# Kernel optimization log

Hardware: AMD Instinct MI355X
Metric: run time of the kernel (lower is better)

Reference implementation:

```python
import jax, jax.numpy as jnp
import numpy as np

B, N, C = 8, 2048, 128
K = 16
DILATIONS = (1, 2)
KMAX = K * max(DILATIONS)  # neighbors constructed by DilatedKnnGraph
NEG_SLOPE = 0.2


def setup_inputs() -> dict:
    key = jax.random.key(0)
    ks = jax.random.split(key, 12)
    D = len(DILATIONS)

    def nrm(k, shape, fan_in):
        return jax.random.normal(k, shape, jnp.float32) / np.float32(np.sqrt(fan_in))

    x = jax.random.normal(ks[0], (B, N, C), jnp.float32)
    pos = jax.random.normal(ks[1], (B, N, 3), jnp.float32)
    # PointTransformerConv params per dilation layer (bias-free lin/lin_src/lin_dst, pos_nn=Linear(3,C))
    W_lin = nrm(ks[2], (D, C, C), C)
    W_src = nrm(ks[3], (D, C, C), C)
    W_dst = nrm(ks[4], (D, C, C), C)
    W_pos = nrm(ks[5], (D, 3, C), 3)
    b_pos = jnp.zeros((D, C), jnp.float32)
    # global fusion MLP: Linear(C+3, C) + LeakyReLU(0.2)
    Wg = nrm(ks[6], (C + 3, C), C + 3)
    bg = jnp.zeros((C,), jnp.float32)
    # final MLP: Linear(C,C) + LeakyReLU(0.2) + Linear(C,3)
    W1 = nrm(ks[7], (C, C), C)
    b1 = jnp.zeros((C,), jnp.float32)
    W2 = nrm(ks[8], (C, 3), C)
    b2 = jnp.zeros((3,), jnp.float32)
    return dict(x=x, pos=pos, W_lin=W_lin, W_src=W_src, W_dst=W_dst,
                W_pos=W_pos, b_pos=b_pos, Wg=Wg, bg=bg, W1=W1, b1=b1, W2=W2, b2=b2)


def _knn(p):
    # p: [N, 3] -> [N, KMAX] neighbor indices sorted by ascending distance (self excluded)
    sq = jnp.sum(p * p, axis=-1)
    d2 = sq[:, None] + sq[None, :] - 2.0 * (p @ p.T)
    d2 = d2 + jnp.eye(p.shape[0], dtype=p.dtype) * jnp.float32(1e10)
    _, idx = jax.lax.top_k(-d2, KMAX)
    return idx


def reference(x, pos, W_lin, W_src, W_dst, W_pos, b_pos, Wg, bg, W1, b1, W2, b2):
    nbr = jax.vmap(_knn)(pos)  # [B, N, KMAX]
    self_idx = jnp.broadcast_to(jnp.arange(N)[None, :, None], (B, N, 1))
    gather = jax.vmap(lambda arr, idx: arr[idx])  # per-cloud fancy gather

    h = None
    for li, d in enumerate(DILATIONS):
        # Dilated neighbor selection: every d-th of sorted neighbors, keep K, plus self loop
        idx = jnp.concatenate([nbr[:, :, ::d][:, :, :K], self_idx], axis=-1)  # [B, N, K+1]
        pos_j = gather(pos, idx)  # [B, N, K+1, 3]
        # delta_ij = pos_nn(pos_i - pos_j)
        delta = jnp.einsum('bnkt,tc->bnkc', pos[:, :, None, :] - pos_j, W_pos[li]) + b_pos[li]
        s = x @ W_src[li]   # lin_src
        v = x @ W_lin[li]   # value projection
        t = x @ W_dst[li]   # lin_dst
        # alpha_ij = lin_dst(x_i) - lin_src(x_j) + delta ; per-channel softmax over neighbors
        alpha = t[:, :, None, :] - gather(s, idx) + delta  # [B, N, K+1, C]
        w = jax.nn.softmax(alpha, axis=2)
        h_ = jnp.sum(w * (gather(v, idx) + delta), axis=2)  # [B, N, C]
        h = h_ if h is None else h + h_

    h2 = jax.nn.leaky_relu(jnp.concatenate([x, pos], axis=-1) @ Wg + bg, NEG_SLOPE)
    h = h + h2
    res = jax.nn.leaky_relu(h @ W1 + b1, NEG_SLOPE) @ W2 + b2
    return res + pos  # add_points=True
```

## Files before the change

### kernel.cpp

```cpp
#include <hip/hip_runtime.h>

#define BB 8
#define NN 2048
#define CC 128
#define KMAX 32
#define NEG 0.2f
#define CH 8
#define CHSZ (NN / CH)
#define CAP 32

using bf16x8 = __attribute__((ext_vector_type(8))) short;
using f32x4  = __attribute__((ext_vector_type(4))) float;

__device__ __forceinline__ unsigned int f2key(float f) {
  unsigned int b = __float_as_uint(f);
  return (b & 0x80000000u) ? ~b : (b | 0x80000000u);
}

__device__ __forceinline__ float sq3(float x, float y, float z) {
  return __fadd_rn(__fadd_rn(__fmul_rn(x, x), __fmul_rn(y, y)), __fmul_rn(z, z));
}

__device__ __forceinline__ float d2np(float px, float py, float pz, float sqq,
                                      float qx, float qy, float qz, float sqj) {
  float dot = __fmaf_rn(pz, qz, __fmaf_rn(py, qy, __fmul_rn(px, qx)));
  return __fsub_rn(__fadd_rn(sqq, sqj), __fmul_rn(2.0f, dot));
}

__device__ __forceinline__ unsigned short f2bf(float f) {
  unsigned int u = __float_as_uint(f);
  return (unsigned short)((u + 0x7fffu + ((u >> 16) & 1u)) >> 16);
}
__device__ __forceinline__ float bf2f(unsigned short u) {
  return __uint_as_float(((unsigned int)u) << 16);
}

__device__ __forceinline__ bf16x8 cvt8(const float* __restrict__ p) {
  float4 a = *(const float4*)(p);
  float4 b = *(const float4*)(p + 4);
  bf16x8 r;
  r[0] = (short)f2bf(a.x); r[1] = (short)f2bf(a.y);
  r[2] = (short)f2bf(a.z); r[3] = (short)f2bf(a.w);
  r[4] = (short)f2bf(b.x); r[5] = (short)f2bf(b.y);
  r[6] = (short)f2bf(b.z); r[7] = (short)f2bf(b.w);
  return r;
}

__device__ __forceinline__ int paddr(int c, int jj) { return (c << 8) + (jj ^ c); }

__device__ __forceinline__ void knn_body(int bx, int tid,
                                         const float* __restrict__ pos,
                                         unsigned short* __restrict__ cand,
                                         unsigned int* __restrict__ candk,
                                         float4* __restrict__ sp4,
                                         unsigned char* __restrict__ sbuf) {
  int b = bx >> 6;
  int qbase = (bx & 63) * 32;
  const float* pb = pos + (size_t)b * NN * 3;
  for (int t = tid; t < NN; t += 256) {
    float xx = pb[t * 3 + 0];
    float yy = pb[t * 3 + 1];
    float zz = pb[t * 3 + 2];
    sp4[paddr(t >> 8, t & 255)] = make_float4(xx, yy, zz, sq3(xx, yy, zz));
  }
  __syncthreads();

  int q = qbase + (tid >> 3);
  int c = tid & 7;
  float4 pq = sp4[paddr(q >> 8, q & 255)];
  float px = pq.x, py = pq.y, pz = pq.z;
  float sqq = pq.w;
  int j0 = c * CHSZ;

  const float SENT = 3.0e38f;
  float a0 = SENT, a1 = SENT, a2 = SENT, a3 = SENT;
#pragma unroll 4
  for (int jj = 0; jj < CHSZ; ++jj) {
    float4 pj = sp4[paddr(c, jj)];
    float d2 = d2np(px, py, pz, sqq, pj.x, pj.y, pj.z, pj.w);
    if (j0 + jj == q) d2 = SENT;
    float m0 = fmaxf(a0, d2); a0 = fminf(a0, d2);
    float m1 = fmaxf(a1, m0); a1 = fminf(a1, m0);
    float m2 = fmaxf(a2, m1); a2 = fminf(a2, m1);
    a3 = fminf(a3, m2);
  }

  float T = a3;
  T = fmaxf(T, __shfl_xor(T, 1));
  T = fmaxf(T, __shfl_xor(T, 2));
  T = fmaxf(T, __shfl_xor(T, 4));

  unsigned int ak[KMAX];
  int ai[KMAX];
#pragma unroll
  for (int k = 0; k < KMAX; ++k) { ak[k] = 0xFFFFFFFFu; ai[k] = 0xFFFF; }

  int sbase = tid * CAP;
  auto drain = [&](int cnt2) {
    for (int u = 0; u < cnt2; ++u) {
      int jj2 = (int)sbuf[sbase + u];
      int j = j0 + jj2;
      float4 pj = sp4[paddr(c, jj2)];
      float d2 = d2np(px, py, pz, sqq, pj.x, pj.y, pj.z, pj.w);
      unsigned int key = f2key(d2);
      if (key < ak[KMAX - 1]) {
#pragma unroll
        for (int k = KMAX - 1; k >= 1; --k) {
          bool ck  = key < ak[k];
          bool ckm = key < ak[k - 1];
          unsigned int tk = ckm ? ak[k - 1] : key;
          int          ti = ckm ? ai[k - 1] : j;
          ak[k] = ck ? tk : ak[k];
          ai[k] = ck ? ti : ai[k];
        }
        bool c0b = key < ak[0];
        ak[0] = c0b ? key : ak[0];
        ai[0] = c0b ? j : ai[0];
      }
    }
  };

  int cnt = 0;
  for (int jj = 0; jj < CHSZ; ++jj) {
    float4 pj = sp4[paddr(c, jj)];
    float d2 = d2np(px, py, pz, sqq, pj.x, pj.y, pj.z, pj.w);
    bool pass = (d2 <= T) && (j0 + jj != q);
    if (pass) {
      if (cnt == CAP) { drain(CAP); cnt = 0; }
      sbuf[sbase + cnt] = (unsigned char)jj;
      ++cnt;
    }
  }
  drain(cnt);

  size_t obase = (((size_t)(b * NN + q)) * CH + c) * KMAX;
  unsigned short* oc = cand + obase;
  unsigned int* ok = candk + obase;
#pragma unroll
  for (int k = 0; k < KMAX; ++k) {
    oc[k] = (unsigned short)ai[k];
    ok[k] = ak[k];
  }
}

__device__ __forceinline__ void proj_body(int z, int mx, int tid,
                                          const float* __restrict__ x,
                                          const unsigned short* __restrict__ wf,
                                          unsigned short* __restrict__ projb) {
  unsigned short* out = projb + (size_t)z * ((size_t)BB * NN * CC);
  int wave = tid >> 6;
  int lane = tid & 63;
  int m0 = (mx * 4 + wave) * 16;
  int quad = lane >> 4;
  int am = m0 + (lane & 15);

  f32x4 acc[8];
#pragma unroll
  for (int nt = 0; nt < 8; ++nt) acc[nt] = (f32x4){0.f, 0.f, 0.f, 0.f};

  const unsigned short* wz = wf + (size_t)z * (8 * 4 * 64 * 8);
#pragma unroll
  for (int ks = 0; ks < 4; ++ks) {
    bf16x8 a = cvt8(x + (size_t)am * CC + ks * 32 + quad * 8);
#pragma unroll
    for (int nt = 0; nt < 8; ++nt) {
      bf16x8 bfr = *(const bf16x8*)(wz + (size_t)(((nt * 4 + ks) * 64 + lane) * 8));
      acc[nt] = __builtin_amdgcn_mfma_f32_16x16x32_bf16(a, bfr, acc[nt], 0, 0, 0);
    }
  }

  int col0 = lane & 15;
#pragma unroll
  for (int nt = 0; nt < 8; ++nt)
#pragma unroll
    for (int r = 0; r < 4; ++r)
      out[(size_t)(m0 + quad * 4 + r) * CC + nt * 16 + col0] = f2bf(acc[nt][r]);
}

__device__ __forceinline__ void wg_body(int mx, int tid,
                                        const float* __restrict__ x,
                                        const float* __restrict__ pos,
                                        const unsigned short* __restrict__ wf,
                                        const float* __restrict__ wgtail,
                                        const float* __restrict__ bg,
                                        float* __restrict__ h) {
  int wave = tid >> 6;
  int lane = tid & 63;
  int m0 = (mx * 4 + wave) * 16;
  int quad = lane >> 4;
  int am = m0 + (lane & 15);

  f32x4 acc[8];
#pragma unroll
  for (int nt = 0; nt < 8; ++nt) acc[nt] = (f32x4){0.f, 0.f, 0.f, 0.f};

  const unsigned short* wz = wf + (size_t)6 * (8 * 4 * 64 * 8);
#pragma unroll
  for (int ks = 0; ks < 4; ++ks) {
    bf16x8 a = cvt8(x + (size_t)am * CC + ks * 32 + quad * 8);
#pragma unroll
    for (int nt = 0; nt < 8; ++nt) {
      bf16x8 b = *(const bf16x8*)(wz + (size_t)(((nt * 4 + ks) * 64 + lane) * 8));
      acc[nt] = __builtin_amdgcn_mfma_f32_16x16x32_bf16(a, b, acc[nt], 0, 0, 0);
    }
  }

  float posr[4][3];
#pragma unroll
  for (int r = 0; r < 4; ++r) {
    int m = m0 + quad * 4 + r;
    posr[r][0] = pos[m * 3 + 0];
    posr[r][1] = pos[m * 3 + 1];
    posr[r][2] = pos[m * 3 + 2];
  }

  int col0 = lane & 15;
#pragma unroll
  for (int nt = 0; nt < 8; ++nt) {
    int col = nt * 16 + col0;
    float bv = bg[col];
    float t0 = wgtail[col];
    float t1 = wgtail[CC + col];
    float t2 = wgtail[2 * CC + col];
#pragma unroll
    for (int r = 0; r < 4; ++r) {
      float v = acc[nt][r] + bv
              + posr[r][0] * t0 + posr[r][1] * t1 + posr[r][2] * t2;
      v = v > 0.f ? v : NEG * v;
      h[(size_t)(m0 + quad * 4 + r) * CC + col] = v;
    }
  }
}

__global__ __launch_bounds__(256) void fused_front(
    const float* __restrict__ pos,
    unsigned short* __restrict__ cand,
    unsigned int* __restrict__ candk,
    const float* __restrict__ x,
    const unsigned short* __restrict__ wf,
    unsigned short* __restrict__ projb,
    const float* __restrict__ wgtail,
    const float* __restrict__ bg,
    float* __restrict__ h) {
  __shared__ float4 sp4[CH * 256];
  __shared__ unsigned char sbuf[256 * CAP];

  if (blockIdx.x < 512) {
    knn_body(blockIdx.x, threadIdx.x, pos, cand, candk, sp4, sbuf);
  } else if (blockIdx.x < 2048) {
    int bx = blockIdx.x - 512;
    proj_body(bx >> 8, bx & 255, threadIdx.x, x, wf, projb);
  } else {
    wg_body(blockIdx.x - 2048, threadIdx.x, x, pos, wf, wgtail, bg, h);
  }
}

__global__ __launch_bounds__(256) void knn_p1(const float* __restrict__ pos,
                                              unsigned short* __restrict__ cand,
                                              unsigned int* __restrict__ candk) {
  __shared__ float4 sp4[CH * 256];
  __shared__ unsigned char sbuf[256 * CAP];
  knn_body(blockIdx.x, threadIdx.x, pos, cand, candk, sp4, sbuf);
}

__global__ __launch_bounds__(64) void knn_p2(const unsigned int* __restrict__ candk,
                                             const unsigned short* __restrict__ cand,
                                             int* __restrict__ nbr) {
  int q = blockIdx.x * 64 + threadIdx.x;
  const unsigned int* k8 = candk + (size_t)q * (CH * KMAX);
  const unsigned short* i8 = cand + (size_t)q * (CH * KMAX);

  int head[CH];
  unsigned int hk[CH];
#pragma unroll
  for (int c = 0; c < CH; ++c) {
    head[c] = 0;
    hk[c] = k8[c * KMAX];
  }

  int* onb = nbr + (size_t)q * KMAX;
#pragma unroll
  for (int r = 0; r < KMAX; ++r) {
    int bc = 0;
    unsigned int bk = hk[0];
#pragma unroll
    for (int c = 1; c < CH; ++c) {
      if (hk[c] < bk) { bk = hk[c]; bc = c; }
    }
    onb[r] = (int)i8[bc * KMAX + head[bc]];
    ++head[bc];
    hk[bc] = (head[bc] < KMAX) ? k8[bc * KMAX + head[bc]] : 0xFFFFFFFFu;
  }
}

__global__ __launch_bounds__(256) void wcvt(const float* __restrict__ Wa,
                                            const float* __restrict__ Wb,
                                            const float* __restrict__ Wc,
                                            const float* __restrict__ Wgm,
                                            const float* __restrict__ W1m,
                                            unsigned short* __restrict__ wf) {
  int t = blockIdx.x * 256 + threadIdx.x;
  int lane = t & 63;
  int ks = (t >> 6) & 3;
  int nt = (t >> 8) & 7;
  int z = t >> 11;
  const float* W = (z < 2) ? (Wa + (size_t)z * CC * CC)
                 : (z < 4) ? (Wb + (size_t)(z - 2) * CC * CC)
                 : (z < 6) ? (Wc + (size_t)(z - 4) * CC * CC)
                 : (z == 6) ? Wgm : W1m;
  int n = nt * 16 + (lane & 15);
  int kb = ks * 32 + (lane >> 4) * 8;
  unsigned short* o = wf + (size_t)t * 8;
#pragma unroll
  for (int j = 0; j < 8; ++j)
    o[j] = f2bf(W[(size_t)(kb + j) * CC + n]);
}

__global__ __launch_bounds__(256) void proj_fly(const float* __restrict__ x,
                                                const unsigned short* __restrict__ wf,
                                                unsigned short* __restrict__ projb) {
  proj_body(blockIdx.z, blockIdx.x, threadIdx.x, x, wf, projb);
}
__global__ __launch_bounds__(256) void wg_fly(const float* __restrict__ x,
                                              const float* __restrict__ pos,
                                              const unsigned short* __restrict__ wf,
                                              const float* __restrict__ wgtail,
                                              const float* __restrict__ bg,
                                              float* __restrict__ h) {
  wg_body(blockIdx.x, threadIdx.x, x, pos, wf, wgtail, bg, h);
}

__global__ __launch_bounds__(128) void attn2_kernel(
    const float* __restrict__ pos, const int* __restrict__ nbr,
    const unsigned short* __restrict__ s0, const unsigned short* __restrict__ v0,
    const unsigned short* __restrict__ t0,
    const unsigned short* __restrict__ s1, const unsigned short* __restrict__ v1,
    const unsigned short* __restrict__ t1,
    const float* __restrict__ Wpos, const float* __restrict__ bpos,
    const float* __restrict__ h, unsigned short* __restrict__ hb) {
  int b = blockIdx.x & 7;
  int n = blockIdx.x >> 3;
  int bn = (b << 11) + n;
  int c = threadIdx.x;

  const float* pb = pos + (size_t)b * NN * 3;
  float pix = pb[n * 3 + 0], piy = pb[n * 3 + 1], piz = pb[n * 3 + 2];
  const int* nb = nbr + (size_t)bn * KMAX;

  float ht = h[(size_t)bn * CC + c];

#pragma unroll
  for (int l = 0; l < 2; ++l) {
    int dil = l + 1;
    const unsigned short* s = l ? s1 : s0;
    const unsigned short* v = l ? v1 : v0;
    const unsigned short* t = l ? t1 : t0;
    const float* Wp = Wpos + (size_t)l * 3 * CC;
    float w0 = Wp[c], w1 = Wp[CC + c], w2 = Wp[2 * CC + c];
    float bp = bpos[(size_t)l * CC + c];
    float tc = bf2f(t[(size_t)bn * CC + c]);

    float alpha[17], del[17];
    float mx = -1e30f;
#pragma unroll
    for (int j = 0; j < 17; ++j) {
      int idx = (j < 16) ? nb[j * dil] : n;
      float dx = pix - pb[idx * 3 + 0];
      float dy = piy - pb[idx * 3 + 1];
      float dz = piz - pb[idx * 3 + 2];
      float d = dx * w0 + dy * w1 + dz * w2 + bp;
      del[j] = d;
      float sc = bf2f(s[((size_t)(b * NN + idx)) * CC + c]);
      float a = tc - sc + d;
      alpha[j] = a;
      mx = fmaxf(mx, a);
    }
    float sum = 0.f;
#pragma unroll
    for (int j = 0; j < 17; ++j) {
      float w = __expf(alpha[j] - mx);
      alpha[j] = w;
      sum += w;
    }
    float inv = 1.f / sum;
    float hc = 0.f;
#pragma unroll
    for (int j = 0; j < 17; ++j) {
      int idx = (j < 16) ? nb[j * dil] : n;
      float vc = bf2f(v[((size_t)(b * NN + idx)) * CC + c]);
      hc += alpha[j] * (vc + del[j]);
    }
    ht += hc * inv;
  }

  hb[(size_t)bn * CC + c] = f2bf(ht);
}

__global__ __launch_bounds__(256) void mfma_w1_final(
    const unsigned short* __restrict__ hb,
    const unsigned short* __restrict__ wz,
    const float* __restrict__ b1,
    const float* __restrict__ W2,
    const float* __restrict__ b2,
    const float* __restrict__ pos,
    float* __restrict__ out) {
  int wave = threadIdx.x >> 6;
  int lane = threadIdx.x & 63;
  int m0 = (blockIdx.x * 4 + wave) * 16;
  int quad = lane >> 4;
  int am = m0 + (lane & 15);

  f32x4 acc[8];
#pragma unroll
  for (int nt = 0; nt < 8; ++nt) acc[nt] = (f32x4){0.f, 0.f, 0.f, 0.f};

#pragma unroll
  for (int ks = 0; ks < 4; ++ks) {
    bf16x8 a = *(const bf16x8*)(hb + (size_t)am * CC + ks * 32 + quad * 8);
#pragma unroll
    for (int nt = 0; nt < 8; ++nt) {
      bf16x8 b = *(const bf16x8*)(wz + (size_t)(((nt * 4 + ks) * 64 + lane) * 8));
      acc[nt] = __builtin_amdgcn_mfma_f32_16x16x32_bf16(a, b, acc[nt], 0, 0, 0);
    }
  }

  int col0 = lane & 15;
  float part[4][3];
#pragma unroll
  for (int r = 0; r < 4; ++r)
#pragma unroll
    for (int d = 0; d < 3; ++d) part[r][d] = 0.f;

#pragma unroll
  for (int nt = 0; nt < 8; ++nt) {
    int col = nt * 16 + col0;
    float bv = b1[col];
    float w20 = W2[col * 3 + 0];
    float w21 = W2[col * 3 + 1];
    float w22 = W2[col * 3 + 2];
#pragma unroll
    for (int r = 0; r < 4; ++r) {
      float gv = acc[nt][r] + bv;
      gv = gv > 0.f ? gv : NEG * gv;
      part[r][0] = fmaf(gv, w20, part[r][0]);
      part[r][1] = fmaf(gv, w21, part[r][1]);
      part[r][2] = fmaf(gv, w22, part[r][2]);
    }
  }

#pragma unroll
  for (int off = 8; off >= 1; off >>= 1) {
#pragma unroll
    for (int r = 0; r < 4; ++r)
#pragma unroll
      for (int d = 0; d < 3; ++d)
        part[r][d] += __shfl_xor(part[r][d], off);
  }

  if (col0 == 0) {
#pragma unroll
    for (int r = 0; r < 4; ++r) {
      int m = m0 + quad * 4 + r;
#pragma unroll
      for (int d = 0; d < 3; ++d)
        out[(size_t)m * 3 + d] = part[r][d] + b2[d] + pos[(size_t)m * 3 + d];
    }
  }
}

extern "C" void kernel_launch(void* const* d_in, const int* in_sizes, int n_in,
                              void* d_out, int out_size, void* d_ws, size_t ws_size,
                              hipStream_t stream) {
  const float* x     = (const float*)d_in[0];
  const float* pos   = (const float*)d_in[1];
  const float* W_lin = (const float*)d_in[2];
  const float* W_src = (const float*)d_in[3];
  const float* W_dst = (const float*)d_in[4];
  const float* W_pos = (const float*)d_in[5];
  const float* b_pos = (const float*)d_in[6];
  const float* Wg    = (const float*)d_in[7];
  const float* bg    = (const float*)d_in[8];
  const float* W1    = (const float*)d_in[9];
  const float* b1    = (const float*)d_in[10];
  const float* W2    = (const float*)d_in[11];
  const float* b2    = (const float*)d_in[12];
  float* out = (float*)d_out;

  const size_t M = (size_t)BB * NN;
  const size_t MC = M * CC;

  char* ws = (char*)d_ws;
  int* nbr = (int*)ws;
  unsigned short* cand = (unsigned short*)(ws + M * KMAX * sizeof(int));
  float* fb = (float*)(ws + M * KMAX * sizeof(int) + M * CH * KMAX * sizeof(unsigned short));
  unsigned short* projb = (unsigned short*)fb;
  unsigned short* sb0 = projb + 0 * MC;
  unsigned short* sb1 = projb + 1 * MC;
  unsigned short* vb0 = projb + 2 * MC;
  unsigned short* vb1 = projb + 3 * MC;
  unsigned short* tb0 = projb + 4 * MC;
  unsigned short* tb1 = projb + 5 * MC;
  unsigned int* candk = (unsigned int*)(fb + 3 * MC);
  float* h = fb + 5 * MC;

  const size_t BASE = M * KMAX * sizeof(int) + M * CH * KMAX * sizeof(unsigned short)
                    + 8 * MC * sizeof(float);
  const size_t XB_BYTES = MC * sizeof(unsigned short);
  const size_t WF_BYTES = 8 * 16384 * sizeof(unsigned short);
  const size_t FRAG = (size_t)(8 * 4 * 64 * 8);
  bool fused_ok = ws_size >= BASE + XB_BYTES + WF_BYTES;

  if (fused_ok) {
    unsigned short* hb = (unsigned short*)(ws + BASE);
    unsigned short* wf = (unsigned short*)(ws + BASE + XB_BYTES);

    wcvt<<<64, 256, 0, stream>>>(W_src, W_lin, W_dst, Wg, W1, wf);
    fused_front<<<2304, 256, 0, stream>>>(pos, cand, candk, x, wf, projb,
                                          Wg + 128 * CC, bg, h);
    knn_p2<<<256, 64, 0, stream>>>(candk, cand, nbr);
    attn2_kernel<<<M, 128, 0, stream>>>(pos, nbr, sb0, vb0, tb0,
                                        sb1, vb1, tb1, W_pos, b_pos, h, hb);
    mfma_w1_final<<<M / 64, 256, 0, stream>>>(hb, wf + 7 * FRAG, b1,
                                              W2, b2, pos, out);
  } else {
    unsigned short* hb = cand;
    unsigned short* wf = cand + MC;
    knn_p1<<<512, 256, 0, stream>>>(pos, cand, candk);
    knn_p2<<<256, 64, 0, stream>>>(candk, cand, nbr);
    wcvt<<<64, 256, 0, stream>>>(W_src, W_lin, W_dst, Wg, W1, wf);
    proj_fly<<<dim3(256, 1, 6), 256, 0, stream>>>(x, wf, projb);
    wg_fly<<<256, 256, 0, stream>>>(x, pos, wf, Wg + 128 * CC, bg, h);
    attn2_kernel<<<M, 128, 0, stream>>>(pos, nbr, sb0, vb0, tb0,
                                        sb1, vb1, tb1, W_pos, b_pos, h, hb);
    mfma_w1_final<<<M / 64, 256, 0, stream>>>(hb, wf + 7 * FRAG, b1,
                                              W2, b2, pos, out);
  }
}
```

Measured before the change: 218.2 us.

## Read kNN points from a precomputed global float4 buffer instead of LDS staging

Adds a small pos4cvt kernel that packs positions with their squared norms into a global float4 array. The kNN body then reads candidate points from global memory (wave-uniform, so broadcast loads) instead of staging the whole cloud in LDS. Threads are remapped so a wave covers 32 queries across two chunks, and the chunk-threshold reduction moves from shuffles to a shared-memory pass with a barrier. This cuts LDS use and the per-block staging work, which may raise occupancy, but it adds a kernel launch and puts the inner-loop loads on the cache path.

```diff
diff --git a/kernel.cpp b/kernel.cpp
--- a/kernel.cpp
+++ b/kernel.cpp
@@ -46,49 +46,55 @@
   return r;
 }
 
-__device__ __forceinline__ int paddr(int c, int jj) { return (c << 8) + (jj ^ c); }
+__global__ __launch_bounds__(256) void pos4cvt(const float* __restrict__ pos,
+                                               float4* __restrict__ pos4) {
+  int t = blockIdx.x * 256 + threadIdx.x;
+  float x = pos[t * 3 + 0];
+  float y = pos[t * 3 + 1];
+  float z = pos[t * 3 + 2];
+  pos4[t] = make_float4(x, y, z, sq3(x, y, z));
+}
 
 __device__ __forceinline__ void knn_body(int bx, int tid,
-                                         const float* __restrict__ pos,
+                                         const float4* __restrict__ pos4,
                                          unsigned short* __restrict__ cand,
                                          unsigned int* __restrict__ candk,
-                                         float4* __restrict__ sp4,
+                                         float* __restrict__ sredT,
                                          unsigned char* __restrict__ sbuf) {
   int b = bx >> 6;
   int qbase = (bx & 63) * 32;
-  const float* pb = pos + (size_t)b * NN * 3;
-  for (int t = tid; t < NN; t += 256) {
-    float xx = pb[t * 3 + 0];
-    float yy = pb[t * 3 + 1];
-    float zz = pb[t * 3 + 2];
-    sp4[paddr(t >> 8, t & 255)] = make_float4(xx, yy, zz, sq3(xx, yy, zz));
-  }
-  __syncthreads();
-
-  int q = qbase + (tid >> 3);
-  int c = tid & 7;
-  float4 pq = sp4[paddr(q >> 8, q & 255)];
+  const float4* pp = pos4 + (size_t)b * NN;
+
+  int lane = tid & 63;
+  int c = ((tid >> 6) << 1) + (lane >> 5);
+  int qi = lane & 31;
+  int q = qbase + qi;
+  int j0 = c * CHSZ;
+
+  float4 pq = pp[q];
   float px = pq.x, py = pq.y, pz = pq.z;
   float sqq = pq.w;
-  int j0 = c * CHSZ;
 
   const float SENT = 3.0e38f;
+  int selfjj = ((q >> 8) == c) ? (q & 255) : 1024;
+
   float a0 = SENT, a1 = SENT, a2 = SENT, a3 = SENT;
 #pragma unroll 4
   for (int jj = 0; jj < CHSZ; ++jj) {
-    float4 pj = sp4[paddr(c, jj)];
+    float4 pj = pp[j0 + jj];
     float d2 = d2np(px, py, pz, sqq, pj.x, pj.y, pj.z, pj.w);
-    if (j0 + jj == q) d2 = SENT;
+    if (jj == selfjj) d2 = SENT;
     float m0 = fmaxf(a0, d2); a0 = fminf(a0, d2);
     float m1 = fmaxf(a1, m0); a1 = fminf(a1, m0);
     float m2 = fmaxf(a2, m1); a2 = fminf(a2, m1);
     a3 = fminf(a3, m2);
   }
 
-  float T = a3;
-  T = fmaxf(T, __shfl_xor(T, 1));
-  T = fmaxf(T, __shfl_xor(T, 2));
-  T = fmaxf(T, __shfl_xor(T, 4));
+  sredT[c * 32 + qi] = a3;
+  __syncthreads();
+  float T = sredT[qi];
+#pragma unroll
+  for (int cc = 1; cc < 8; ++cc) T = fmaxf(T, sredT[cc * 32 + qi]);
 
   unsigned int ak[KMAX];
   int ai[KMAX];
@@ -100,7 +106,7 @@
     for (int u = 0; u < cnt2; ++u) {
       int jj2 = (int)sbuf[sbase + u];
       int j = j0 + jj2;
-      float4 pj = sp4[paddr(c, jj2)];
+      float4 pj = pp[j];
       float d2 = d2np(px, py, pz, sqq, pj.x, pj.y, pj.z, pj.w);
       unsigned int key = f2key(d2);
       if (key < ak[KMAX - 1]) {
@@ -122,9 +128,9 @@
 
   int cnt = 0;
   for (int jj = 0; jj < CHSZ; ++jj) {
-    float4 pj = sp4[paddr(c, jj)];
+    float4 pj = pp[j0 + jj];
     float d2 = d2np(px, py, pz, sqq, pj.x, pj.y, pj.z, pj.w);
-    bool pass = (d2 <= T) && (j0 + jj != q);
+    bool pass = (d2 <= T) && (jj != selfjj);
     if (pass) {
       if (cnt == CAP) { drain(CAP); cnt = 0; }
       sbuf[sbase + cnt] = (unsigned char)jj;
@@ -234,6 +240,7 @@
 
 __global__ __launch_bounds__(256) void fused_front(
     const float* __restrict__ pos,
+    const float4* __restrict__ pos4,
     unsigned short* __restrict__ cand,
     unsigned int* __restrict__ candk,
     const float* __restrict__ x,
@@ -242,11 +249,11 @@
     const float* __restrict__ wgtail,
     const float* __restrict__ bg,
     float* __restrict__ h) {
-  __shared__ float4 sp4[CH * 256];
+  __shared__ float sredT[256];
   __shared__ unsigned char sbuf[256 * CAP];
 
   if (blockIdx.x < 512) {
-    knn_body(blockIdx.x, threadIdx.x, pos, cand, candk, sp4, sbuf);
+    knn_body(blockIdx.x, threadIdx.x, pos4, cand, candk, sredT, sbuf);
   } else if (blockIdx.x < 2048) {
     int bx = blockIdx.x - 512;
     proj_body(bx >> 8, bx & 255, threadIdx.x, x, wf, projb);
@@ -255,12 +262,12 @@
   }
 }
 
-__global__ __launch_bounds__(256) void knn_p1(const float* __restrict__ pos,
+__global__ __launch_bounds__(256) void knn_p1(const float4* __restrict__ pos4,
                                               unsigned short* __restrict__ cand,
                                               unsigned int* __restrict__ candk) {
-  __shared__ float4 sp4[CH * 256];
+  __shared__ float sredT[256];
   __shared__ unsigned char sbuf[256 * CAP];
-  knn_body(blockIdx.x, threadIdx.x, pos, cand, candk, sp4, sbuf);
+  knn_body(blockIdx.x, threadIdx.x, pos4, cand, candk, sredT, sbuf);
 }
 
 __global__ __launch_bounds__(64) void knn_p2(const unsigned int* __restrict__ candk,
@@ -502,6 +509,7 @@
   unsigned short* tb1 = projb + 5 * MC;
   unsigned int* candk = (unsigned int*)(fb + 3 * MC);
   float* h = fb + 5 * MC;
+  float4* pos4 = (float4*)(fb + 6 * MC);
 
   const size_t BASE = M * KMAX * sizeof(int) + M * CH * KMAX * sizeof(unsigned short)
                     + 8 * MC * sizeof(float);
@@ -515,7 +523,8 @@
     unsigned short* wf = (unsigned short*)(ws + BASE + XB_BYTES);
 
     wcvt<<<64, 256, 0, stream>>>(W_src, W_lin, W_dst, Wg, W1, wf);
-    fused_front<<<2304, 256, 0, stream>>>(pos, cand, candk, x, wf, projb,
+    pos4cvt<<<64, 256, 0, stream>>>(pos, pos4);
+    fused_front<<<2304, 256, 0, stream>>>(pos, pos4, cand, candk, x, wf, projb,
                                           Wg + 128 * CC, bg, h);
     knn_p2<<<256, 64, 0, stream>>>(candk, cand, nbr);
     attn2_kernel<<<M, 128, 0, stream>>>(pos, nbr, sb0, vb0, tb0,
@@ -525,7 +534,8 @@
   } else {
     unsigned short* hb = cand;
     unsigned short* wf = cand + MC;
-    knn_p1<<<512, 256, 0, stream>>>(pos, cand, candk);
+    pos4cvt<<<64, 256, 0, stream>>>(pos, pos4);
+    knn_p1<<<512, 256, 0, stream>>>(pos4, cand, candk);
     knn_p2<<<256, 64, 0, stream>>>(candk, cand, nbr);
     wcvt<<<64, 256, 0, stream>>>(W_src, W_lin, W_dst, Wg, W1, wf);
     proj_fly<<<dim3(256, 1, 6), 256, 0, stream>>>(x, wf, projb);
```

Result: slower. 253.6 us (+16.2%).
